# Optimization experiments

Measured on AMD Instinct MI355X. Metric: run time of the kernel, lower is better.

## Reference

```python
import jax, jax.numpy as jnp
import numpy as np


def setup_inputs() -> dict:
    key = jax.random.key(0)
    k1, k2, k3 = jax.random.split(key, 3)
    B, N, D = 8, 4096, 64
    q = jax.random.normal(k1, (B, N, D), dtype=jnp.float32)
    k = jax.random.normal(k2, (B, N, D), dtype=jnp.float32)
    v = jax.random.normal(k3, (B, N, D), dtype=jnp.float32)
    attn_mask = jnp.ones((B, N), dtype=jnp.int32)  # 1 = attend, 0 = padding
    return {"q": q, "k": k, "v": v, "attn_mask": attn_mask}


def reference(q, k, v, attn_mask):
    # q: [B, n_q, d], k/v: [B, n_k, d], attn_mask: [B, n_k]
    d = q.shape[-1]
    n_q, n_k = q.shape[1], k.shape[1]
    scale = jnp.sqrt(jnp.asarray(d, dtype=q.dtype))
    # [B, n_q, n_k] attention logits
    logits = jnp.einsum("bqd,bkd->bqk", q, k) / scale
    # causal (mask_future=True): tril keep-mask over (n_q, n_k)
    causal = jnp.tril(jnp.ones((n_q, n_k), dtype=bool))
    neg_inf = jnp.asarray(-jnp.inf, dtype=logits.dtype)
    logits = jnp.where(causal[None, :, :], logits, neg_inf)
    # padding mask broadcast over query dim: [B, 1, n_k]
    logits = jnp.where(attn_mask[:, None, :] == 0, neg_inf, logits)
    w = jax.nn.softmax(logits, axis=-1)
    return jnp.einsum("bqk,bkd->bqd", w, v)
```

## Files before the change

kernel.cpp:

```cpp
#include <hip/hip_runtime.h>


#define BATCH 8
#define SEQ   4096
#define DIM   64
#define QT    64
#define NKT   (SEQ / 64)

typedef __attribute__((ext_vector_type(8))) short bf16x8;
typedef __attribute__((ext_vector_type(4))) float f32x4;

__device__ inline short f2bf(float f) {
    unsigned u = __builtin_bit_cast(unsigned, f);
    u += 0x7FFFu + ((u >> 16) & 1u);
    return (short)(u >> 16);
}

__device__ inline unsigned pk2bf(float a, float b) {
    unsigned ua = __builtin_bit_cast(unsigned, a) + 0x8000u;
    unsigned ub = __builtin_bit_cast(unsigned, b) + 0x8000u;
    return __builtin_amdgcn_perm(ub, ua, 0x07060302u);
}

__device__ inline float fast_exp2(float x) {
#if __has_builtin(__builtin_amdgcn_exp2f)
    return __builtin_amdgcn_exp2f(x);
#else
    return exp2f(x);
#endif
}

__device__ inline void gl_lds16(const void* g, void* l) {
    __builtin_amdgcn_global_load_lds(
        (const __attribute__((address_space(1))) void*)g,
        (__attribute__((address_space(3))) void*)l, 16, 0, 0);
}

__global__ __launch_bounds__(256)
void prep_kv(const float* __restrict__ kg, const float* __restrict__ vg,
             short* __restrict__ kw, short* __restrict__ vw) {
    const int tile = blockIdx.x;
    const float* kp = kg + (size_t)tile * 64 * DIM;
    const float* vp = vg + (size_t)tile * 64 * DIM;
    short* ko = kw + (size_t)tile * 4096;
    short* vo = vw + (size_t)tile * 4096;
    const int t = threadIdx.x;
#pragma unroll
    for (int i = 0; i < 4; ++i) {
        const int flat = i * 256 + t;
        const int key = flat >> 4, d0 = (flat & 15) * 4;
        const float4 kv = *(const float4*)(kp + (size_t)key * DIM + d0);
        uint2 kpk;
        kpk.x = pk2bf(kv.x, kv.y); kpk.y = pk2bf(kv.z, kv.w);
        *(uint2*)(ko + (((d0 >> 3) << 6) + key) * 8 + (d0 & 7)) = kpk;
        const float4 vv = *(const float4*)(vp + (size_t)key * DIM + d0);
        const int kc = key >> 3, jk = key & 7;
        vo[((kc << 6) + d0 + 0) * 8 + jk] = f2bf(vv.x);
        vo[((kc << 6) + d0 + 1) * 8 + jk] = f2bf(vv.y);
        vo[((kc << 6) + d0 + 2) * 8 + jk] = f2bf(vv.z);
        vo[((kc << 6) + d0 + 3) * 8 + jk] = f2bf(vv.w);
    }
}

template <bool WS>
__global__ __launch_bounds__(512, 4)
void attn_fwd(const float* __restrict__ qg, const float* __restrict__ kg,
              const float* __restrict__ vg, const int* __restrict__ mg,
              float* __restrict__ og, const short* __restrict__ kw,
              const short* __restrict__ vw) {
    __shared__ __align__(16) char smem[59392];
    short* KbS = (short*)smem;
    short* VbS = (short*)(smem + 16384);
    short* PbS = (short*)(smem + 32768);
    float* Ml  = (float*)(smem + 43008);
    float* OX = (float*)smem;
    float* LB = (float*)(smem + 16384);

    const int t    = threadIdx.x;
    const int w    = t >> 6;
    const int L    = t & 63;
    const int c15  = L & 15;
    const int quad = L >> 4;
    const int qsub = w & 3;
    const int kh   = w >> 2;

    const int id = blockIdx.x;
    const int b  = id & 7;
    const int j  = id >> 3;
    const int qb = (j < 32) ? (63 - j) : (j - 32);
    const int qbase  = qb * QT;
    const int ntiles = qb + 1;

    const float* qp = qg + (size_t)b * SEQ * DIM;
    const float* kp = kg + (size_t)b * SEQ * DIM;
    const float* vp = vg + (size_t)b * SEQ * DIM;
    const int*   mp = mg + (size_t)b * SEQ;
    const short* kwb = WS ? kw + (size_t)b * NKT * 4096 : nullptr;
    const short* vwb = WS ? vw + (size_t)b * NKT * 4096 : nullptr;

    const int qrow = qbase + qsub * 16 + c15;
    const float qscale = 0.125f * 1.44269504088896340736f;

    bf16x8 Qf[2];
#pragma unroll
    for (int c = 0; c < 2; ++c) {
        const float* src = qp + (size_t)qrow * DIM + c * 32 + quad * 8;
        float4 x = *(const float4*)(src);
        float4 y = *(const float4*)(src + 4);
        bf16x8 f;
        f[0] = f2bf(x.x * qscale); f[1] = f2bf(x.y * qscale);
        f[2] = f2bf(x.z * qscale); f[3] = f2bf(x.w * qscale);
        f[4] = f2bf(y.x * qscale); f[5] = f2bf(y.y * qscale);
        f[6] = f2bf(y.z * qscale); f[7] = f2bf(y.w * qscale);
        Qf[c] = f;
    }

    auto stage = [&](int bs, int kt) {
        const short* ks = kwb + (size_t)kt * 4096;
        const short* vs = vwb + (size_t)kt * 4096;
        const int off = w << 9;
        gl_lds16(ks + off + (L << 3), KbS + bs * 4096 + off);
        gl_lds16(vs + off + (L << 3), VbS + bs * 4096 + off);
    };

    for (int i = t; i < ntiles * 64; i += 512)
        Ml[i] = mp[i] ? 0.0f : -1e30f;

    float lsum = 0.0f;
    f32x4 Oacc[4];
#pragma unroll
    for (int nb = 0; nb < 4; ++nb) Oacc[nb] = (f32x4){0.f, 0.f, 0.f, 0.f};

    if constexpr (WS) stage(0, 0);

    short* Pw = PbS + w * 640;

    for (int kt = 0; kt < ntiles; ++kt) {
        const int cur = WS ? (kt & 1) : 0;

        if constexpr (!WS) {
            __syncthreads();
#pragma unroll
            for (int it = 0; it < 2; ++it) {
                const int flat = it * 512 + t;
                const int key = flat >> 4, d0 = (flat & 15) * 4;
                const float4 kv = *(const float4*)(kp + (size_t)(kt * 64 + key) * DIM + d0);
                uint2 kk;
                kk.x = pk2bf(kv.x, kv.y); kk.y = pk2bf(kv.z, kv.w);
                *(uint2*)&KbS[(((d0 >> 3) << 6) + key) * 8 + (d0 & 7)] = kk;
                const float4 vv = *(const float4*)(vp + (size_t)(kt * 64 + key) * DIM + d0);
                const int kc = key >> 3, jk = key & 7;
                VbS[((kc << 6) + d0 + 0) * 8 + jk] = f2bf(vv.x);
                VbS[((kc << 6) + d0 + 1) * 8 + jk] = f2bf(vv.y);
                VbS[((kc << 6) + d0 + 2) * 8 + jk] = f2bf(vv.z);
                VbS[((kc << 6) + d0 + 3) * 8 + jk] = f2bf(vv.w);
            }
            __syncthreads();
        } else {
            __syncthreads();
            if (kt + 1 < ntiles) stage(cur ^ 1, kt + 1);
        }

        const short* Kt = KbS + cur * 4096;
        const short* Vt = VbS + cur * 4096;

        f32x4 sacc[2];
        sacc[0] = (f32x4){0.f, 0.f, 0.f, 0.f};
        sacc[1] = (f32x4){0.f, 0.f, 0.f, 0.f};
#pragma unroll
        for (int c = 0; c < 2; ++c) {
#pragma unroll
            for (int i = 0; i < 2; ++i) {
                bf16x8 kf = *(const bf16x8*)&Kt[(((quad + 4 * c) << 6) + (2 * kh + i) * 16 + c15) * 8];
                sacc[i] = __builtin_amdgcn_mfma_f32_16x16x32_bf16(kf, Qf[c], sacc[i], 0, 0, 0);
            }
        }

        const bool diag = (kt == ntiles - 1);
#pragma unroll
        for (int i = 0; i < 2; ++i) {
            const int kb = 2 * kh + i;
            const float4 ma = *(const float4*)&Ml[kt * 64 + kb * 16 + quad * 4];
            const float mar[4] = {ma.x, ma.y, ma.z, ma.w};
            float p[4];
#pragma unroll
            for (int r = 0; r < 4; ++r) {
                float s = sacc[i][r] + mar[r];
                if (diag) {
                    const int keyg = kt * 64 + kb * 16 + quad * 4 + r;
                    if (keyg > qrow) s = -1e30f;
                }
                p[r] = fast_exp2(fminf(s, 80.0f));
                lsum += p[r];
            }
            uint2 pp;
            pp.x = pk2bf(p[0], p[1]);
            pp.y = pk2bf(p[2], p[3]);
            *(uint2*)&Pw[c15 * 40 + i * 16 + quad * 4] = pp;
        }

        bf16x8 pf = *(const bf16x8*)&Pw[c15 * 40 + quad * 8];
#pragma unroll
        for (int nb = 0; nb < 4; ++nb) {
            bf16x8 vf = *(const bf16x8*)&Vt[(((kh * 4 + quad) << 6) + nb * 16 + c15) * 8];
            Oacc[nb] = __builtin_amdgcn_mfma_f32_16x16x32_bf16(pf, vf, Oacc[nb], 0, 0, 0);
        }
    }

    lsum += __shfl_xor(lsum, 16);
    lsum += __shfl_xor(lsum, 32);

    __syncthreads();
    if (w >= 4) {
        const int g = w & 3;
#pragma unroll
        for (int r = 0; r < 4; ++r) {
            const int q = quad * 4 + r;
#pragma unroll
            for (int nb = 0; nb < 4; ++nb)
                OX[(g * 16 + q) * 64 + nb * 16 + c15] = Oacc[nb][r];
        }
        if (quad == 0) LB[g * 16 + c15] = lsum;
    }
    __syncthreads();
    if (w < 4) {
        const float inv = 1.0f / (lsum + LB[w * 16 + c15]);
        float* op = og + (size_t)b * SEQ * DIM;
#pragma unroll
        for (int r = 0; r < 4; ++r) {
            const float ir = __shfl(inv, (L & 48) + ((L & 48) >> 2) + r);
            const int row = qbase + w * 16 + quad * 4 + r;
#pragma unroll
            for (int nb = 0; nb < 4; ++nb)
                op[(size_t)row * DIM + nb * 16 + c15] =
                    (Oacc[nb][r] + OX[(w * 16 + quad * 4 + r) * 64 + nb * 16 + c15]) * ir;
        }
    }
}

extern "C" void kernel_launch(void* const* d_in, const int* in_sizes, int n_in,
                              void* d_out, int out_size, void* d_ws, size_t ws_size,
                              hipStream_t stream) {
    (void)in_sizes; (void)n_in; (void)out_size;
    const float* q = (const float*)d_in[0];
    const float* k = (const float*)d_in[1];
    const float* v = (const float*)d_in[2];
    const int*   m = (const int*)d_in[3];
    float* o = (float*)d_out;
    const size_t need = (size_t)BATCH * NKT * 4096 * sizeof(short) * 2;
    if (ws_size >= need) {
        short* kw = (short*)d_ws;
        short* vw = kw + (size_t)BATCH * NKT * 4096;
        prep_kv<<<dim3(BATCH * NKT), 256, 0, stream>>>(k, v, kw, vw);
        attn_fwd<true><<<dim3(512), 512, 0, stream>>>(q, k, v, m, o, kw, vw);
    } else {
        attn_fwd<false><<<dim3(512), 512, 0, stream>>>(q, k, v, m, o, nullptr, nullptr);
    }
}
```

Before: 131.5 us.

## Switch attention to 32x32 MFMA with register double-buffered K/V loads

Rewrites the attention kernel around 32x32x16 bf16 MFMA tiles with 256-thread blocks. Each wave now loads pre-packed K/V fragments and mask values straight from global memory into registers, double-buffered one tile ahead, so the LDS staging and per-tile barriers go away. P is rearranged into MFMA operand layout with cross-lane shuffles rather than an LDS round trip. The epilogue stages output through padded LDS so it can be written with coalesced float4 stores. The trade-off is that waves sharing a key half now fetch the same K/V twice from cache, and register pressure is higher.

```diff
diff --git a/kernel.cpp b/kernel.cpp
--- a/kernel.cpp
+++ b/kernel.cpp
@@ -4,24 +4,22 @@
 #define BATCH 8
 #define SEQ   4096
 #define DIM   64
-#define QT    64
 #define NKT   (SEQ / 64)
 
-typedef __attribute__((ext_vector_type(8))) short bf16x8;
-typedef __attribute__((ext_vector_type(4))) float f32x4;
+typedef __attribute__((ext_vector_type(8)))  short bf16x8;
+typedef __attribute__((ext_vector_type(4)))  float f32x4;
+typedef __attribute__((ext_vector_type(16))) float f32x16;
 
 __device__ inline short f2bf(float f) {
     unsigned u = __builtin_bit_cast(unsigned, f);
     u += 0x7FFFu + ((u >> 16) & 1u);
     return (short)(u >> 16);
 }
-
 __device__ inline unsigned pk2bf(float a, float b) {
     unsigned ua = __builtin_bit_cast(unsigned, a) + 0x8000u;
     unsigned ub = __builtin_bit_cast(unsigned, b) + 0x8000u;
     return __builtin_amdgcn_perm(ub, ua, 0x07060302u);
 }
-
 __device__ inline float fast_exp2(float x) {
 #if __has_builtin(__builtin_amdgcn_exp2f)
     return __builtin_amdgcn_exp2f(x);
@@ -29,11 +27,11 @@
     return exp2f(x);
 #endif
 }
-
-__device__ inline void gl_lds16(const void* g, void* l) {
-    __builtin_amdgcn_global_load_lds(
-        (const __attribute__((address_space(1))) void*)g,
-        (__attribute__((address_space(3))) void*)l, 16, 0, 0);
+__device__ inline bf16x8 pack8(const float4& a, const float4& b) {
+    bf16x8 r;
+    r[0] = f2bf(a.x); r[1] = f2bf(a.y); r[2] = f2bf(a.z); r[3] = f2bf(a.w);
+    r[4] = f2bf(b.x); r[5] = f2bf(b.y); r[6] = f2bf(b.z); r[7] = f2bf(b.w);
+    return r;
 }
 
 __global__ __launch_bounds__(256)
@@ -63,32 +61,27 @@
 }
 
 template <bool WS>
-__global__ __launch_bounds__(512, 4)
+__global__ __launch_bounds__(256, 2)
 void attn_fwd(const float* __restrict__ qg, const float* __restrict__ kg,
               const float* __restrict__ vg, const int* __restrict__ mg,
               float* __restrict__ og, const short* __restrict__ kw,
               const short* __restrict__ vw) {
-    __shared__ __align__(16) char smem[59392];
-    short* KbS = (short*)smem;
-    short* VbS = (short*)(smem + 16384);
-    short* PbS = (short*)(smem + 32768);
-    float* Ml  = (float*)(smem + 43008);
-    float* OX = (float*)smem;
-    float* LB = (float*)(smem + 16384);
+    __shared__ float Ob[2][32 * 65];
+    __shared__ float Lb[2][32];
 
     const int t    = threadIdx.x;
     const int w    = t >> 6;
     const int L    = t & 63;
-    const int c15  = L & 15;
-    const int quad = L >> 4;
-    const int qsub = w & 3;
-    const int kh   = w >> 2;
+    const int q31  = L & 31;
+    const int h    = L >> 5;
+    const int kh   = w & 1;
+    const int qsub = w >> 1;
 
     const int id = blockIdx.x;
     const int b  = id & 7;
     const int j  = id >> 3;
-    const int qb = (j < 32) ? (63 - j) : (j - 32);
-    const int qbase  = qb * QT;
+    const int qb = 63 - 2 * (j & 31) - (j >> 5);
+    const int qbase  = qb * 64;
     const int ntiles = qb + 1;
 
     const float* qp = qg + (size_t)b * SEQ * DIM;
@@ -98,142 +91,154 @@
     const short* kwb = WS ? kw + (size_t)b * NKT * 4096 : nullptr;
     const short* vwb = WS ? vw + (size_t)b * NKT * 4096 : nullptr;
 
-    const int qrow = qbase + qsub * 16 + c15;
+    const int qrow = qbase + qsub * 32 + q31;
     const float qscale = 0.125f * 1.44269504088896340736f;
 
-    bf16x8 Qf[2];
-#pragma unroll
-    for (int c = 0; c < 2; ++c) {
-        const float* src = qp + (size_t)qrow * DIM + c * 32 + quad * 8;
-        float4 x = *(const float4*)(src);
+    bf16x8 Qf[4];
+#pragma unroll
+    for (int c = 0; c < 4; ++c) {
+        const float* src = qp + (size_t)qrow * DIM + c * 16 + h * 8;
+        float4 x = *(const float4*)src;
         float4 y = *(const float4*)(src + 4);
-        bf16x8 f;
-        f[0] = f2bf(x.x * qscale); f[1] = f2bf(x.y * qscale);
-        f[2] = f2bf(x.z * qscale); f[3] = f2bf(x.w * qscale);
-        f[4] = f2bf(y.x * qscale); f[5] = f2bf(y.y * qscale);
-        f[6] = f2bf(y.z * qscale); f[7] = f2bf(y.w * qscale);
-        Qf[c] = f;
-    }
-
-    auto stage = [&](int bs, int kt) {
-        const short* ks = kwb + (size_t)kt * 4096;
-        const short* vs = vwb + (size_t)kt * 4096;
-        const int off = w << 9;
-        gl_lds16(ks + off + (L << 3), KbS + bs * 4096 + off);
-        gl_lds16(vs + off + (L << 3), VbS + bs * 4096 + off);
+        x.x *= qscale; x.y *= qscale; x.z *= qscale; x.w *= qscale;
+        y.x *= qscale; y.y *= qscale; y.z *= qscale; y.w *= qscale;
+        Qf[c] = pack8(x, y);
+    }
+
+    float lsum = 0.0f;
+    f32x16 Oacc[2];
+#pragma unroll
+    for (int nb = 0; nb < 2; ++nb)
+#pragma unroll
+        for (int r = 0; r < 16; ++r) Oacc[nb][r] = 0.0f;
+
+    auto loadt = [&](bf16x8 (&Kd)[4], bf16x8 (&Vd)[4], int4 (&Md)[4], int kt) {
+        if constexpr (WS) {
+            const short* kb = kwb + (size_t)kt * 4096;
+            const short* vb = vwb + (size_t)kt * 4096;
+#pragma unroll
+            for (int c = 0; c < 4; ++c)
+                Kd[c] = *(const bf16x8*)&kb[(((2 * c + h) << 6) + kh * 32 + q31) * 8];
+#pragma unroll
+            for (int kk = 0; kk < 2; ++kk)
+#pragma unroll
+                for (int nb = 0; nb < 2; ++nb)
+                    Vd[kk * 2 + nb] = *(const bf16x8*)&vb[(((4 * kh + 2 * kk + h) << 6) + nb * 32 + q31) * 8];
+        } else {
+#pragma unroll
+            for (int c = 0; c < 4; ++c) {
+                const float* src = kp + (size_t)(kt * 64 + kh * 32 + q31) * DIM + c * 16 + h * 8;
+                Kd[c] = pack8(*(const float4*)src, *(const float4*)(src + 4));
+            }
+#pragma unroll
+            for (int kk = 0; kk < 2; ++kk)
+#pragma unroll
+                for (int nb = 0; nb < 2; ++nb) {
+                    bf16x8 f;
+#pragma unroll
+                    for (int jj = 0; jj < 8; ++jj)
+                        f[jj] = f2bf(vp[(size_t)(kt * 64 + kh * 32 + 16 * kk + 8 * h + jj) * DIM + nb * 32 + q31]);
+                    Vd[kk * 2 + nb] = f;
+                }
+        }
+#pragma unroll
+        for (int g = 0; g < 4; ++g)
+            Md[g] = *(const int4*)&mp[kt * 64 + kh * 32 + 8 * g + 4 * h];
     };
 
-    for (int i = t; i < ntiles * 64; i += 512)
-        Ml[i] = mp[i] ? 0.0f : -1e30f;
-
-    float lsum = 0.0f;
-    f32x4 Oacc[4];
-#pragma unroll
-    for (int nb = 0; nb < 4; ++nb) Oacc[nb] = (f32x4){0.f, 0.f, 0.f, 0.f};
-
-    if constexpr (WS) stage(0, 0);
-
-    short* Pw = PbS + w * 640;
-
-    for (int kt = 0; kt < ntiles; ++kt) {
-        const int cur = WS ? (kt & 1) : 0;
-
-        if constexpr (!WS) {
-            __syncthreads();
-#pragma unroll
-            for (int it = 0; it < 2; ++it) {
-                const int flat = it * 512 + t;
-                const int key = flat >> 4, d0 = (flat & 15) * 4;
-                const float4 kv = *(const float4*)(kp + (size_t)(kt * 64 + key) * DIM + d0);
-                uint2 kk;
-                kk.x = pk2bf(kv.x, kv.y); kk.y = pk2bf(kv.z, kv.w);
-                *(uint2*)&KbS[(((d0 >> 3) << 6) + key) * 8 + (d0 & 7)] = kk;
-                const float4 vv = *(const float4*)(vp + (size_t)(kt * 64 + key) * DIM + d0);
-                const int kc = key >> 3, jk = key & 7;
-                VbS[((kc << 6) + d0 + 0) * 8 + jk] = f2bf(vv.x);
-                VbS[((kc << 6) + d0 + 1) * 8 + jk] = f2bf(vv.y);
-                VbS[((kc << 6) + d0 + 2) * 8 + jk] = f2bf(vv.z);
-                VbS[((kc << 6) + d0 + 3) * 8 + jk] = f2bf(vv.w);
-            }
-            __syncthreads();
-        } else {
-            __syncthreads();
-            if (kt + 1 < ntiles) stage(cur ^ 1, kt + 1);
-        }
-
-        const short* Kt = KbS + cur * 4096;
-        const short* Vt = VbS + cur * 4096;
-
-        f32x4 sacc[2];
-        sacc[0] = (f32x4){0.f, 0.f, 0.f, 0.f};
-        sacc[1] = (f32x4){0.f, 0.f, 0.f, 0.f};
-#pragma unroll
-        for (int c = 0; c < 2; ++c) {
-#pragma unroll
-            for (int i = 0; i < 2; ++i) {
-                bf16x8 kf = *(const bf16x8*)&Kt[(((quad + 4 * c) << 6) + (2 * kh + i) * 16 + c15) * 8];
-                sacc[i] = __builtin_amdgcn_mfma_f32_16x16x32_bf16(kf, Qf[c], sacc[i], 0, 0, 0);
+    auto compute = [&](bf16x8 (&Kc)[4], bf16x8 (&Vc)[4], int4 (&Mc)[4], int kt) {
+        f32x16 sa;
+#pragma unroll
+        for (int r = 0; r < 16; ++r) sa[r] = 0.0f;
+#pragma unroll
+        for (int c = 0; c < 4; ++c)
+            sa = __builtin_amdgcn_mfma_f32_32x32x16_bf16(Kc[c], Qf[c], sa, 0, 0, 0);
+
+        const bool diag = (kt == ntiles - 1);
+        float p[16];
+#pragma unroll
+        for (int g = 0; g < 4; ++g) {
+            const int mi[4] = {Mc[g].x, Mc[g].y, Mc[g].z, Mc[g].w};
+#pragma unroll
+            for (int e = 0; e < 4; ++e) {
+                const int reg = g * 4 + e;
+                float s = sa[reg];
+                bool keep = (mi[e] != 0);
+                if (diag) {
+                    const int keyg = kt * 64 + kh * 32 + 4 * h + e + 8 * g;
+                    keep = keep && (keyg <= qrow);
+                }
+                s = keep ? s : -1e30f;
+                p[reg] = fast_exp2(fminf(s, 80.0f));
+                lsum += p[reg];
             }
         }
 
-        const bool diag = (kt == ntiles - 1);
-#pragma unroll
-        for (int i = 0; i < 2; ++i) {
-            const int kb = 2 * kh + i;
-            const float4 ma = *(const float4*)&Ml[kt * 64 + kb * 16 + quad * 4];
-            const float mar[4] = {ma.x, ma.y, ma.z, ma.w};
-            float p[4];
-#pragma unroll
-            for (int r = 0; r < 4; ++r) {
-                float s = sacc[i][r] + mar[r];
-                if (diag) {
-                    const int keyg = kt * 64 + kb * 16 + quad * 4 + r;
-                    if (keyg > qrow) s = -1e30f;
+        unsigned u[8], su[8];
+#pragma unroll
+        for (int i = 0; i < 8; ++i) u[i] = pk2bf(p[2 * i], p[2 * i + 1]);
+#pragma unroll
+        for (int i = 0; i < 8; ++i) su[i] = (unsigned)__shfl_xor((int)u[i], 32);
+        int4 fi0 = h ? (int4){(int)su[2], (int)su[3], (int)u[2], (int)u[3]}
+                     : (int4){(int)u[0], (int)u[1], (int)su[0], (int)su[1]};
+        int4 fi1 = h ? (int4){(int)su[6], (int)su[7], (int)u[6], (int)u[7]}
+                     : (int4){(int)u[4], (int)u[5], (int)su[4], (int)su[5]};
+        bf16x8 pf0 = __builtin_bit_cast(bf16x8, fi0);
+        bf16x8 pf1 = __builtin_bit_cast(bf16x8, fi1);
+
+        Oacc[0] = __builtin_amdgcn_mfma_f32_32x32x16_bf16(Vc[0], pf0, Oacc[0], 0, 0, 0);
+        Oacc[1] = __builtin_amdgcn_mfma_f32_32x32x16_bf16(Vc[1], pf0, Oacc[1], 0, 0, 0);
+        Oacc[0] = __builtin_amdgcn_mfma_f32_32x32x16_bf16(Vc[2], pf1, Oacc[0], 0, 0, 0);
+        Oacc[1] = __builtin_amdgcn_mfma_f32_32x32x16_bf16(Vc[3], pf1, Oacc[1], 0, 0, 0);
+    };
+
+    bf16x8 K0[4], V0[4], K1[4], V1[4];
+    int4 M0[4], M1[4];
+    loadt(K0, V0, M0, 0);
+    int kt = 0;
+    for (;;) {
+        if (kt + 1 < ntiles) loadt(K1, V1, M1, kt + 1);
+        compute(K0, V0, M0, kt);
+        if (++kt >= ntiles) break;
+        if (kt + 1 < ntiles) loadt(K0, V0, M0, kt + 1);
+        compute(K1, V1, M1, kt);
+        if (++kt >= ntiles) break;
+    }
+
+    lsum += __shfl_xor(lsum, 32);
+
+    if (kh == 1) {
+#pragma unroll
+        for (int nb = 0; nb < 2; ++nb)
+#pragma unroll
+            for (int r = 0; r < 16; ++r)
+                Ob[qsub][((nb * 16 + r) * 2 + h) * 32 + q31] = Oacc[nb][r];
+        if (h == 0) Lb[qsub][q31] = lsum;
+    }
+    __syncthreads();
+    if (kh == 0) {
+        const float inv = 1.0f / (lsum + Lb[qsub][q31]);
+#pragma unroll
+        for (int nb = 0; nb < 2; ++nb)
+#pragma unroll
+            for (int r = 0; r < 16; ++r)
+                Oacc[nb][r] = (Oacc[nb][r] + Ob[qsub][((nb * 16 + r) * 2 + h) * 32 + q31]) * inv;
+#pragma unroll
+        for (int nb = 0; nb < 2; ++nb)
+#pragma unroll
+            for (int g = 0; g < 4; ++g)
+#pragma unroll
+                for (int e = 0; e < 4; ++e) {
+                    const int d = nb * 32 + 4 * h + 8 * g + e;
+                    Ob[qsub][q31 * 65 + d] = Oacc[nb][g * 4 + e];
                 }
-                p[r] = fast_exp2(fminf(s, 80.0f));
-                lsum += p[r];
-            }
-            uint2 pp;
-            pp.x = pk2bf(p[0], p[1]);
-            pp.y = pk2bf(p[2], p[3]);
-            *(uint2*)&Pw[c15 * 40 + i * 16 + quad * 4] = pp;
-        }
-
-        bf16x8 pf = *(const bf16x8*)&Pw[c15 * 40 + quad * 8];
-#pragma unroll
-        for (int nb = 0; nb < 4; ++nb) {
-            bf16x8 vf = *(const bf16x8*)&Vt[(((kh * 4 + quad) << 6) + nb * 16 + c15) * 8];
-            Oacc[nb] = __builtin_amdgcn_mfma_f32_16x16x32_bf16(pf, vf, Oacc[nb], 0, 0, 0);
-        }
-    }
-
-    lsum += __shfl_xor(lsum, 16);
-    lsum += __shfl_xor(lsum, 32);
-
-    __syncthreads();
-    if (w >= 4) {
-        const int g = w & 3;
-#pragma unroll
-        for (int r = 0; r < 4; ++r) {
-            const int q = quad * 4 + r;
-#pragma unroll
-            for (int nb = 0; nb < 4; ++nb)
-                OX[(g * 16 + q) * 64 + nb * 16 + c15] = Oacc[nb][r];
-        }
-        if (quad == 0) LB[g * 16 + c15] = lsum;
-    }
-    __syncthreads();
-    if (w < 4) {
-        const float inv = 1.0f / (lsum + LB[w * 16 + c15]);
         float* op = og + (size_t)b * SEQ * DIM;
 #pragma unroll
-        for (int r = 0; r < 4; ++r) {
-            const float ir = __shfl(inv, (L & 48) + ((L & 48) >> 2) + r);
-            const int row = qbase + w * 16 + quad * 4 + r;
-#pragma unroll
-            for (int nb = 0; nb < 4; ++nb)
-                op[(size_t)row * DIM + nb * 16 + c15] =
-                    (Oacc[nb][r] + OX[(w * 16 + quad * 4 + r) * 64 + nb * 16 + c15]) * ir;
+        for (int i = 0; i < 8; ++i) {
+            const int flat = i * 256 + (L << 2);
+            const int row = flat >> 6, d = flat & 63;
+            const float4 val = *(const float4*)&Ob[qsub][row * 65 + d];
+            *(float4*)&op[(size_t)(qbase + qsub * 32 + row) * DIM + d] = val;
         }
     }
 }
@@ -252,8 +257,8 @@
         short* kw = (short*)d_ws;
         short* vw = kw + (size_t)BATCH * NKT * 4096;
         prep_kv<<<dim3(BATCH * NKT), 256, 0, stream>>>(k, v, kw, vw);
-        attn_fwd<true><<<dim3(512), 512, 0, stream>>>(q, k, v, m, o, kw, vw);
+        attn_fwd<true><<<dim3(512), 256, 0, stream>>>(q, k, v, m, o, kw, vw);
     } else {
-        attn_fwd<false><<<dim3(512), 512, 0, stream>>>(q, k, v, m, o, nullptr, nullptr);
-    }
-}
+        attn_fwd<false><<<dim3(512), 256, 0, stream>>>(q, k, v, m, o, nullptr, nullptr);
+    }
+}
```

New measurement: 161.4 us. +22.7%, slower.
